# Kernel optimization log

Measured on AMD Instinct MI355X. Metric: run time of the kernel, lower is better.

The kernel has to match this reference:

```python
import jax, jax.numpy as jnp
import numpy as np
from jax import lax

MAX_ALPHA = 0.00015
MAX_BETA = 0.00015
NOISE_GRAIN = 0.05
LN_EPS = 1e-5


def gaussian_blur(x, ksize, sigma):
    # depthwise 2D gaussian blur, same padding; x: [B, C, H, W]
    r = ksize // 2
    g = jnp.exp(-(jnp.linspace(-r, r, ksize, dtype=x.dtype) ** 2) / (2.0 * sigma ** 2))
    g = g / g.sum()
    k2d = g[:, None] * g[None, :]                       # [k, k]
    C = x.shape[1]
    kernel = jnp.broadcast_to(k2d, (C, 1, ksize, ksize))  # OIHW, depthwise
    return lax.conv_general_dilated(
        x, kernel, window_strides=(1, 1), padding=[(r, r), (r, r)],
        feature_group_count=C, dimension_numbers=('NCHW', 'OIHW', 'NCHW'))


def setup_inputs() -> dict:
    key = jax.random.key(0)
    ks = jax.random.split(key, 8)
    B, C, H, W = 8, 3, 1024, 1024
    L, D = 1024, 512
    Dh = D // 4
    return {
        'x_bg': jax.random.uniform(ks[0], (B, C, H, W), dtype=jnp.float32),
        'bottleneck_feat': jax.random.normal(ks[1], (B, L, D), dtype=jnp.float32),
        'mask': jax.random.uniform(ks[2], (B, 1, H, W), dtype=jnp.float32),
        'noise': jax.random.normal(ks[3], (B, C, H, W), dtype=jnp.float32),
        'W1': jax.random.normal(ks[4], (D, Dh), dtype=jnp.float32) * (1.0 / np.sqrt(D)),
        'b1': jnp.zeros((Dh,), dtype=jnp.float32),
        'ln_g': jnp.ones((Dh,), dtype=jnp.float32),
        'ln_b': jnp.zeros((Dh,), dtype=jnp.float32),
        'W2': jax.random.normal(ks[5], (Dh, 2), dtype=jnp.float32) * 0.01,
        'b2': jnp.zeros((2,), dtype=jnp.float32),
    }


def reference(x_bg, bottleneck_feat, mask, noise, W1, b1, ln_g, ln_b, W2, b2):
    # param head on global-pooled bottleneck feature
    feat_global = bottleneck_feat.mean(axis=1)                 # [B, D]
    h = feat_global @ W1 + b1                                  # [B, D/4]
    mu = h.mean(axis=-1, keepdims=True)
    var = ((h - mu) ** 2).mean(axis=-1, keepdims=True)
    h = (h - mu) * lax.rsqrt(var + LN_EPS) * ln_g + ln_b
    h = jax.nn.relu(h)
    params = h @ W2 + b2                                       # [B, 2]
    alpha = jax.nn.sigmoid(params[:, 0])[:, None, None, None] * MAX_ALPHA
    beta = jax.nn.sigmoid(params[:, 1])[:, None, None, None] * MAX_BETA

    # synthesize
    variance = alpha * x_bg + beta
    sigma = jnp.sqrt(jnp.maximum(variance, 1e-7))
    n = gaussian_blur(noise, 7, NOISE_GRAIN) * 1.5
    mask_soft = gaussian_blur(mask, 21, 5.0)                   # [B,1,H,W] broadcast
    noisy_output = x_bg + n * sigma * mask_soft
    return noisy_output, alpha, beta
```

## Files before the change

### kernel.cpp

```cpp
#include <hip/hip_runtime.h>
#include <math.h>

#define B 8
#define C 3
#define H 1024
#define W 1024
#define L 1024
#define D 512
#define DH 128
#define NPIX (H * W)
#define NOISY_ELEMS (B * C * NPIX)
#define TH 16
#define RPB 8
#define LROW 1056

typedef float vf2 __attribute__((ext_vector_type(2)));
typedef float vf4 __attribute__((ext_vector_type(4)));

struct BlurW { float w[21]; };

__global__ __launch_bounds__(256) void hblur_colsum_kernel(
        const float* __restrict__ mask, float* __restrict__ hmask,
        const float* __restrict__ feat, float* __restrict__ partial, BlurW kw) {
    int wgid = blockIdx.x;
    int t = threadIdx.x;
    __shared__ float Ls[RPB][LROW];

    if (wgid < 1024) {
        size_t row0 = (size_t)wgid * RPB;
        const float* src = mask + row0 * W;
        #pragma unroll
        for (int r = 0; r < RPB; ++r) {
            vf4 v = __builtin_nontemporal_load((const vf4*)(src + (size_t)r * W) + t);
            *(vf4*)&Ls[r][12 + 4 * t] = v;
        }
        if (t < RPB * 10) {
            int r = t / 10, i = t - 10 * r;
            Ls[r][2 + i] = 0.f;
            Ls[r][12 + W + i] = 0.f;
        }
        __syncthreads();
        float* dst = hmask + row0 * W;
        #pragma unroll
        for (int r = 0; r < RPB; ++r) {
            float v[28];
            #pragma unroll
            for (int j = 0; j < 7; ++j) {
                vf4 q = *(const vf4*)&Ls[r][4 * t + 4 * j];
                v[4 * j] = q.x; v[4 * j + 1] = q.y; v[4 * j + 2] = q.z; v[4 * j + 3] = q.w;
            }
            vf4 o;
            #pragma unroll
            for (int i = 0; i < 4; ++i) {
                float acc = 0.f;
                #pragma unroll
                for (int k = 0; k < 10; ++k)
                    acc = fmaf(kw.w[k], v[i + 2 + k] + v[i + 22 - k], acc);
                o[i] = fmaf(kw.w[10], v[i + 12], acc);
            }
            __builtin_nontemporal_store(o, (vf4*)(dst + (size_t)r * W) + t);
        }
    } else {
        int blk = wgid - 1024;
        int b = blk >> 5, chunk = blk & 31;
        int d4 = (t & 127) * 4;
        int half = t >> 7;
        const float* base = feat + (size_t)b * (L * D)
                          + (size_t)(chunk * 32 + half * 16) * D + d4;
        vf4 s = {0.f, 0.f, 0.f, 0.f};
        #pragma unroll
        for (int ll = 0; ll < 16; ++ll) {
            vf4 v = *(const vf4*)(base + (size_t)ll * D);
            s.x += v.x; s.y += v.y; s.z += v.z; s.w += v.w;
        }
        float* dst = partial + ((size_t)(b * 64 + chunk * 2 + half)) * 512 + d4;
        *(vf4*)dst = s;
    }
}

__global__ void head_kernel(const float* __restrict__ partial,
                            const float* __restrict__ W1, const float* __restrict__ b1,
                            const float* __restrict__ ln_g, const float* __restrict__ ln_b,
                            const float* __restrict__ W2, const float* __restrict__ b2,
                            float* __restrict__ ab, float* __restrict__ out_tail) {
    const int b = blockIdx.x;
    const int j = threadIdx.x;
    __shared__ float fm[D];
    __shared__ float red[DH];
    for (int d = j; d < D; d += DH) {
        float s = 0.f;
        const float* p = partial + (size_t)b * 64 * D + d;
        for (int c = 0; c < 64; ++c) s += p[c * D];
        fm[d] = s * (1.0f / (float)L);
    }
    __syncthreads();
    float h = b1[j];
    const vf4* fm4 = (const vf4*)fm;
    #pragma unroll 8
    for (int d4 = 0; d4 < D / 4; ++d4) {
        vf4 f = fm4[d4];
        h = fmaf(f.x, W1[(4 * d4 + 0) * DH + j], h);
        h = fmaf(f.y, W1[(4 * d4 + 1) * DH + j], h);
        h = fmaf(f.z, W1[(4 * d4 + 2) * DH + j], h);
        h = fmaf(f.w, W1[(4 * d4 + 3) * DH + j], h);
    }

    red[j] = h; __syncthreads();
    for (int s = 64; s > 0; s >>= 1) { if (j < s) red[j] += red[j + s]; __syncthreads(); }
    float mu = red[0] * (1.f / (float)DH);
    __syncthreads();
    float hc = h - mu;
    red[j] = hc * hc; __syncthreads();
    for (int s = 64; s > 0; s >>= 1) { if (j < s) red[j] += red[j + s]; __syncthreads(); }
    float var = red[0] * (1.f / (float)DH);
    __syncthreads();

    float hn = hc * rsqrtf(var + 1e-5f) * ln_g[j] + ln_b[j];
    hn = fmaxf(hn, 0.f);

    red[j] = hn * W2[j * 2 + 0]; __syncthreads();
    for (int s = 64; s > 0; s >>= 1) { if (j < s) red[j] += red[j + s]; __syncthreads(); }
    float p0 = red[0];
    __syncthreads();
    red[j] = hn * W2[j * 2 + 1]; __syncthreads();
    for (int s = 64; s > 0; s >>= 1) { if (j < s) red[j] += red[j + s]; __syncthreads(); }
    float p1 = red[0];

    if (j == 0) {
        float a  = 0.00015f / (1.f + expf(-(p0 + b2[0])));
        float be = 0.00015f / (1.f + expf(-(p1 + b2[1])));
        ab[b] = a; ab[8 + b] = be;
        out_tail[b] = a; out_tail[8 + b] = be;
    }
}

__global__ __launch_bounds__(256) void final_kernel(
        const float* __restrict__ x_bg, const float* __restrict__ noise,
        const float* __restrict__ hmask, const float* __restrict__ ab,
        float* __restrict__ out, BlurW kw) {
    int blk = blockIdx.x;
    int b   = blk >> 7;
    int rem = blk & 127;
    int s   = rem >> 1;
    int wj  = rem & 1;
    int h0  = s * TH;
    int t   = threadIdx.x;
    int x0  = wj * 512 + 2 * t;

    const float* hmb = hmask + (size_t)b * NPIX + x0;
    const vf2 zero2 = {0.f, 0.f};

    vf2 ms[TH];
    #pragma unroll
    for (int r = 0; r < TH; ++r) ms[r] = zero2;

    #pragma unroll
    for (int k = 0; k < TH + 20; ++k) {
        int hy = h0 - 10 + k;
        vf2 wv = (hy >= 0 && hy < H) ? *(const vf2*)(hmb + (size_t)hy * W) : zero2;
        #pragma unroll
        for (int r = 0; r < TH; ++r) {
            int dk = k - r;
            if (dk >= 0 && dk < 21) {
                ms[r].x = fmaf(kw.w[dk], wv.x, ms[r].x);
                ms[r].y = fmaf(kw.w[dk], wv.y, ms[r].y);
            }
        }
    }

    float alpha = ab[b], beta = ab[8 + b];

    #pragma unroll
    for (int c = 0; c < C; ++c) {
        const float* xb = x_bg  + (((size_t)(b * C + c) * H) + h0) * W + x0;
        const float* nb = noise + (((size_t)(b * C + c) * H) + h0) * W + x0;
        float*       ob = out   + (((size_t)(b * C + c) * H) + h0) * W + x0;
        #pragma unroll
        for (int r = 0; r < TH; ++r) {
            vf2 x  = __builtin_nontemporal_load((const vf2*)(xb + (size_t)r * W));
            vf2 nz = __builtin_nontemporal_load((const vf2*)(nb + (size_t)r * W));
            vf2 o;
            float sgx = sqrtf(fmaxf(fmaf(alpha, x.x, beta), 1e-7f));
            float sgy = sqrtf(fmaxf(fmaf(alpha, x.y, beta), 1e-7f));
            o.x = fmaf(1.5f * nz.x * sgx, ms[r].x, x.x);
            o.y = fmaf(1.5f * nz.y * sgy, ms[r].y, x.y);
            *(vf2*)(ob + (size_t)r * W) = o;
        }
    }
}

extern "C" void kernel_launch(void* const* d_in, const int* in_sizes, int n_in,
                              void* d_out, int out_size, void* d_ws, size_t ws_size,
                              hipStream_t stream) {
    const float* x_bg = (const float*)d_in[0];
    const float* feat = (const float*)d_in[1];
    const float* mask = (const float*)d_in[2];
    const float* noise = (const float*)d_in[3];
    const float* W1 = (const float*)d_in[4];
    const float* b1 = (const float*)d_in[5];
    const float* ln_g = (const float*)d_in[6];
    const float* ln_b = (const float*)d_in[7];
    const float* W2 = (const float*)d_in[8];
    const float* b2 = (const float*)d_in[9];
    float* out = (float*)d_out;

    float* ws_f = (float*)d_ws;
    float* partial = ws_f;
    float* ab = ws_f + 262144;
    float* hmask = ws_f + 262144 + 64;

    BlurW kw;
    {
        double g[21], s = 0.0;
        for (int i = 0; i < 21; ++i) { double x = (double)(i - 10); g[i] = exp(-x * x / 50.0); s += g[i]; }
        for (int i = 0; i < 21; ++i) kw.w[i] = (float)(g[i] / s);
    }

    hblur_colsum_kernel<<<1024 + 256, 256, 0, stream>>>(mask, hmask, feat, partial, kw);
    head_kernel<<<B, 128, 0, stream>>>(partial, W1, b1, ln_g, ln_b, W2, b2,
                                       ab, out + NOISY_ELEMS);
    final_kernel<<<B * 64 * 2, 256, 0, stream>>>(x_bg, noise, hmask, ab, out, kw);
}
```

Before: 100.8 us.

## Store horizontally blurred mask as bf16 and use rolling vertical window

```diff
diff --git a/kernel.cpp b/kernel.cpp
--- a/kernel.cpp
+++ b/kernel.cpp
@@ -10,17 +10,24 @@
 #define DH 128
 #define NPIX (H * W)
 #define NOISY_ELEMS (B * C * NPIX)
-#define TH 16
+#define TH 8
 #define RPB 8
 #define LROW 1056
 
 typedef float vf2 __attribute__((ext_vector_type(2)));
 typedef float vf4 __attribute__((ext_vector_type(4)));
+typedef unsigned short us4 __attribute__((ext_vector_type(4)));
 
 struct BlurW { float w[21]; };
 
+static __device__ __forceinline__ unsigned short f2bf(float f) {
+    unsigned u = __float_as_uint(f);
+    u += 0x7FFFu + ((u >> 16) & 1u);
+    return (unsigned short)(u >> 16);
+}
+
 __global__ __launch_bounds__(256) void hblur_colsum_kernel(
-        const float* __restrict__ mask, float* __restrict__ hmask,
+        const float* __restrict__ mask, unsigned short* __restrict__ hmask,
         const float* __restrict__ feat, float* __restrict__ partial, BlurW kw) {
     int wgid = blockIdx.x;
     int t = threadIdx.x;
@@ -40,7 +47,7 @@
             Ls[r][12 + W + i] = 0.f;
         }
         __syncthreads();
-        float* dst = hmask + row0 * W;
+        unsigned short* dst = hmask + row0 * W;
         #pragma unroll
         for (int r = 0; r < RPB; ++r) {
             float v[28];
@@ -49,16 +56,17 @@
                 vf4 q = *(const vf4*)&Ls[r][4 * t + 4 * j];
                 v[4 * j] = q.x; v[4 * j + 1] = q.y; v[4 * j + 2] = q.z; v[4 * j + 3] = q.w;
             }
-            vf4 o;
+            us4 o;
             #pragma unroll
             for (int i = 0; i < 4; ++i) {
                 float acc = 0.f;
                 #pragma unroll
                 for (int k = 0; k < 10; ++k)
                     acc = fmaf(kw.w[k], v[i + 2 + k] + v[i + 22 - k], acc);
-                o[i] = fmaf(kw.w[10], v[i + 12], acc);
+                acc = fmaf(kw.w[10], v[i + 12], acc);
+                o[i] = f2bf(acc);
             }
-            __builtin_nontemporal_store(o, (vf4*)(dst + (size_t)r * W) + t);
+            *(us4*)(dst + (size_t)r * W + 4 * t) = o;
         }
     } else {
         int blk = wgid - 1024;
@@ -136,55 +144,70 @@
 
 __global__ __launch_bounds__(256) void final_kernel(
         const float* __restrict__ x_bg, const float* __restrict__ noise,
-        const float* __restrict__ hmask, const float* __restrict__ ab,
+        const unsigned short* __restrict__ hmask, const float* __restrict__ ab,
         float* __restrict__ out, BlurW kw) {
     int blk = blockIdx.x;
-    int b   = blk >> 7;
-    int rem = blk & 127;
+    int b   = blk >> 8;
+    int rem = blk & 255;
     int s   = rem >> 1;
     int wj  = rem & 1;
     int h0  = s * TH;
     int t   = threadIdx.x;
     int x0  = wj * 512 + 2 * t;
 
-    const float* hmb = hmask + (size_t)b * NPIX + x0;
+    const unsigned short* hmb = hmask + (size_t)b * NPIX + x0;
     const vf2 zero2 = {0.f, 0.f};
 
-    vf2 ms[TH];
+    vf2 win[21];
     #pragma unroll
-    for (int r = 0; r < TH; ++r) ms[r] = zero2;
+    for (int k = 0; k < 21; ++k) {
+        int hy = h0 - 10 + k;
+        if (hy >= 0 && hy < H) {
+            unsigned u = *(const unsigned*)(hmb + (size_t)hy * W);
+            win[k].x = __uint_as_float(u << 16);
+            win[k].y = __uint_as_float(u & 0xFFFF0000u);
+        } else win[k] = zero2;
+    }
+
+    float alpha = ab[b], beta = ab[8 + b];
 
     #pragma unroll
-    for (int k = 0; k < TH + 20; ++k) {
-        int hy = h0 - 10 + k;
-        vf2 wv = (hy >= 0 && hy < H) ? *(const vf2*)(hmb + (size_t)hy * W) : zero2;
-        #pragma unroll
-        for (int r = 0; r < TH; ++r) {
-            int dk = k - r;
-            if (dk >= 0 && dk < 21) {
-                ms[r].x = fmaf(kw.w[dk], wv.x, ms[r].x);
-                ms[r].y = fmaf(kw.w[dk], wv.y, ms[r].y);
-            }
-        }
-    }
-
-    float alpha = ab[b], beta = ab[8 + b];
-
-    #pragma unroll
-    for (int c = 0; c < C; ++c) {
-        const float* xb = x_bg  + (((size_t)(b * C + c) * H) + h0) * W + x0;
-        const float* nb = noise + (((size_t)(b * C + c) * H) + h0) * W + x0;
-        float*       ob = out   + (((size_t)(b * C + c) * H) + h0) * W + x0;
-        #pragma unroll
-        for (int r = 0; r < TH; ++r) {
-            vf2 x  = __builtin_nontemporal_load((const vf2*)(xb + (size_t)r * W));
-            vf2 nz = __builtin_nontemporal_load((const vf2*)(nb + (size_t)r * W));
+    for (int r = 0; r < TH; ++r) {
+        float mx = 0.f, my = 0.f;
+        #pragma unroll
+        for (int k = 0; k < 10; ++k) {
+            float wk = kw.w[k];
+            vf2 v1 = win[(r + k) % 21];
+            vf2 v2 = win[(r + 20 - k) % 21];
+            mx = fmaf(wk, v1.x + v2.x, mx);
+            my = fmaf(wk, v1.y + v2.y, my);
+        }
+        {
+            vf2 vm = win[(r + 10) % 21];
+            mx = fmaf(kw.w[10], vm.x, mx);
+            my = fmaf(kw.w[10], vm.y, my);
+        }
+        int h = h0 + r;
+        #pragma unroll
+        for (int c = 0; c < C; ++c) {
+            size_t idx = (((size_t)(b * C + c) * H) + h) * W + x0;
+            vf2 x = __builtin_nontemporal_load((const vf2*)(x_bg + idx));
+            vf2 nz = __builtin_nontemporal_load((const vf2*)(noise + idx));
             vf2 o;
             float sgx = sqrtf(fmaxf(fmaf(alpha, x.x, beta), 1e-7f));
             float sgy = sqrtf(fmaxf(fmaf(alpha, x.y, beta), 1e-7f));
-            o.x = fmaf(1.5f * nz.x * sgx, ms[r].x, x.x);
-            o.y = fmaf(1.5f * nz.y * sgy, ms[r].y, x.y);
-            *(vf2*)(ob + (size_t)r * W) = o;
+            o.x = fmaf(1.5f * nz.x * sgx, mx, x.x);
+            o.y = fmaf(1.5f * nz.y * sgy, my, x.y);
+            __builtin_nontemporal_store(o, (vf2*)(out + idx));
+        }
+        if (r < TH - 1) {
+            int hy = h0 + r + 11;
+            int slot = r % 21;
+            if (hy < H) {
+                unsigned u = *(const unsigned*)(hmb + (size_t)hy * W);
+                win[slot].x = __uint_as_float(u << 16);
+                win[slot].y = __uint_as_float(u & 0xFFFF0000u);
+            } else win[slot] = zero2;
         }
     }
 }
@@ -207,7 +230,7 @@
     float* ws_f = (float*)d_ws;
     float* partial = ws_f;
     float* ab = ws_f + 262144;
-    float* hmask = ws_f + 262144 + 64;
+    unsigned short* hmask = (unsigned short*)(ws_f + 262144 + 64);
 
     BlurW kw;
     {
@@ -219,5 +242,5 @@
     hblur_colsum_kernel<<<1024 + 256, 256, 0, stream>>>(mask, hmask, feat, partial, kw);
     head_kernel<<<B, 128, 0, stream>>>(partial, W1, b1, ln_g, ln_b, W2, b2,
                                        ab, out + NOISY_ELEMS);
-    final_kernel<<<B * 64 * 2, 256, 0, stream>>>(x_bg, noise, hmask, ab, out, kw);
-}
+    final_kernel<<<2048, 256, 0, stream>>>(x_bg, noise, hmask, ab, out, kw);
+}
```

Result: slower. 104.5 us (+3.7%).
